# Optimization experiments

Measured on AMD Instinct MI355X. Metric: run time of the kernel, lower is better.

## Reference

```python
import jax, jax.numpy as jnp
import numpy as np

EPS = 1e-5
NUM_HEADS = 12

def _ln(x, g, b):
    m = jnp.mean(x, -1, keepdims=True)
    v = jnp.var(x, -1, keepdims=True)
    return (x - m) * jax.lax.rsqrt(v + EPS) * g + b

def setup_inputs():
    key = jax.random.key(0)
    ks = jax.random.split(key, 8)
    D, Dh = 768, 3072
    B, T, H, Wd = 8, 8, 14, 14
    def w(k, shape, scale=0.02):
        return jax.random.normal(k, shape, jnp.float32) * scale
    return dict(
        x=jax.random.normal(ks[0], (B, T * H * Wd + 1, D), jnp.float32),
        W_mq=w(ks[1], (D, D)), b_mq=jnp.zeros((D,), jnp.float32),
        W_mk=w(ks[2], (D, D)), b_mk=jnp.zeros((D,), jnp.float32),
        g1=jnp.ones((D,), jnp.float32), be1=jnp.zeros((D,), jnp.float32),
        W_qkv=w(ks[3], (3 * D, D)),
        W_proj=w(ks[4], (D, D)), b_proj=jnp.zeros((D,), jnp.float32),
        g2=jnp.ones((D,), jnp.float32), be2=jnp.zeros((D,), jnp.float32),
        W_fc1=w(ks[5], (Dh, D)), b_fc1=jnp.zeros((Dh,), jnp.float32),
        W_fc2=w(ks[6], (D, Dh)), b_fc2=jnp.zeros((D,), jnp.float32),
        B=B, T=T, H=H, Wd=Wd,
    )

def reference(x, W_mq, b_mq, W_mk, b_mk, g1, be1, W_qkv, W_proj, b_proj,
              g2, be2, W_fc1, b_fc1, W_fc2, b_fc2, B, T, H, Wd):
    D = x.shape[-1]
    nh = NUM_HEADS
    hd = D // nh
    res = x
    # cls token: (B,1,D) -> repeated per frame -> (B*T,1,D)
    cls = jnp.repeat(x[:, :1, :], T, axis=1).reshape(B * T, 1, D)
    # spatial tokens: 'b (h w t) m -> (b t) (h w) m'  (t is fastest-varying)
    xs = x[:, 1:, :].reshape(B, H * Wd, T, D).transpose(0, 2, 1, 3).reshape(B * T, H * Wd, D)
    xt = jnp.concatenate([cls, xs], axis=1)  # (BT, N=197, D)
    # learned QK-gated mask
    qm = xt @ W_mq.T + b_mq
    km = xt @ W_mk.T + b_mk
    lm = jnp.einsum('bnd,bmd->bnm', qm, km)
    lm = lm.at[:, 0, 0].set(100.0)  # force cls->cls gate open
    lm = jax.nn.sigmoid(lm)
    # attention (drop rates are 0; drop_path is identity at inference)
    xn = _ln(xt, g1, be1)
    BT, N = xt.shape[0], xt.shape[1]
    qkv = (xn @ W_qkv.T).reshape(BT, N, 3, nh, hd).transpose(2, 0, 3, 1, 4)
    q, k, v = qkv[0], qkv[1], qkv[2]  # (BT, nh, N, hd)
    attn = jax.nn.softmax(jnp.einsum('bhnd,bhmd->bhnm', q, k) * (hd ** -0.5), axis=-1)
    attn = attn * lm[:, None, :, :]  # gate attention probs with learned mask
    o = jnp.einsum('bhnm,bhmd->bhnd', attn, v).transpose(0, 2, 1, 3).reshape(BT, N, D)
    o = o @ W_proj.T + b_proj
    # gather cls back (mean over frames) and scatter tokens back
    cls_o = jnp.mean(o[:, 0, :].reshape(B, T, D), axis=1, keepdims=True)  # (B,1,D)
    xs_o = o[:, 1:, :].reshape(B, T, H * Wd, D).transpose(0, 2, 1, 3).reshape(B, H * Wd * T, D)
    y = res + jnp.concatenate([cls_o, xs_o], axis=1)
    # MLP
    h = _ln(y, g2, be2)
    h = jax.nn.gelu(h @ W_fc1.T + b_fc1, approximate=False)
    y = y + (h @ W_fc2.T + b_fc2)
    return (y, lm)
```

## Files before the change

### kernel.cpp

```cpp
#include <hip/hip_runtime.h>
#include <cstdint>

typedef _Float16 f16;
typedef f16 f16x2 __attribute__((ext_vector_type(2)));
typedef f16 f16x4 __attribute__((ext_vector_type(4)));
typedef f16 f16x8 __attribute__((ext_vector_type(8)));
typedef float f32x4 __attribute__((ext_vector_type(4)));

constexpr int D = 768;
constexpr int NTOK = 197;
constexpr int BT = 64;
constexpr int ROWS_A = BT * NTOK;
constexpr int SEQ = 1569;
constexpr int ROWS_Y = 8 * SEQ;
constexpr int DH = 3072;
constexpr int CW = 2304;
constexpr long Y_ELEMS = (long)ROWS_Y * D;

__device__ __forceinline__ void gload_lds16(const f16* g, f16* l) {
  __builtin_amdgcn_global_load_lds(
      (const __attribute__((address_space(1))) void*)g,
      (__attribute__((address_space(3))) void*)l, 16, 0, 0);
}

constexpr int DD4 = D * D / 4;
constexpr int QKV4 = CW * D / 4;
constexpr int FC4 = DH * D / 4;
constexpr int W2_TOT = QKV4 + DD4 + 2 * FC4;

__global__ __launch_bounds__(256) void cvt_weights(
    const float* __restrict__ wqkv_f, const float* __restrict__ wproj_f,
    const float* __restrict__ wfc1_f, const float* __restrict__ wfc2_f,
    f16* __restrict__ wqkv, f16* __restrict__ wproj,
    f16* __restrict__ wfc1, f16* __restrict__ wfc2) {
  const int i = blockIdx.x * 256 + threadIdx.x;
  const float* src;
  f16* dst;
  int j;
  if (i < QKV4) { src = wqkv_f; dst = wqkv; j = i; }
  else if (i < QKV4 + DD4) { src = wproj_f; dst = wproj; j = i - QKV4; }
  else if (i < QKV4 + DD4 + FC4) { src = wfc1_f; dst = wfc1; j = i - QKV4 - DD4; }
  else if (i < W2_TOT) { src = wfc2_f; dst = wfc2; j = i - QKV4 - DD4 - FC4; }
  else return;
  const float4 v = *(const float4*)(src + (size_t)j * 4);
  f16x4 o = {(f16)v.x, (f16)v.y, (f16)v.z, (f16)v.w};
  *(f16x4*)(dst + (size_t)j * 4) = o;
}

__global__ __launch_bounds__(256) void transpose2_f16(
    const float* __restrict__ wq, const float* __restrict__ wk,
    f16* __restrict__ wqT, f16* __restrict__ wkT) {
  __shared__ float tile[32][33];
  const int bid = blockIdx.x;
  const int bx = bid % 24, by = (bid / 24) % 24, z = bid / 576;
  const float* src = z ? wk : wq;
  f16* dst = z ? wkT : wqT;
  const int tx = threadIdx.x & 31, ty4 = (threadIdx.x >> 5) * 4;
#pragma unroll
  for (int r = 0; r < 4; r++)
    tile[ty4 + r][tx] = src[(size_t)(by * 32 + ty4 + r) * D + bx * 32 + tx];
  __syncthreads();
#pragma unroll
  for (int r = 0; r < 4; r++)
    dst[(size_t)(bx * 32 + ty4 + r) * D + by * 32 + tx] = (f16)tile[tx][ty4 + r];
}

__global__ __launch_bounds__(256) void weight_prep(
    const float* __restrict__ wq, const float* __restrict__ wk,
    const float* __restrict__ bq, const float* __restrict__ bk,
    float* __restrict__ rq, float* __restrict__ rk, float* __restrict__ beta) {
  const int tid = blockIdx.x * 256 + threadIdx.x;
  if (tid < D) {
    float s = 0.f;
    for (int k = 0; k < D; k++) s += wq[(size_t)k * D + tid] * bk[k];
    rq[tid] = s;
  } else if (tid < 2 * D) {
    const int i = tid - D;
    float s = 0.f;
    for (int k = 0; k < D; k++) s += wk[(size_t)k * D + i] * bq[k];
    rk[i] = s;
  }
  if (blockIdx.x == 0 && threadIdx.x < 64) {
    float c = 0.f;
    for (int k = threadIdx.x; k < D; k += 64) c += bq[k] * bk[k];
    for (int off = 32; off; off >>= 1) c += __shfl_xor(c, off);
    if (threadIdx.x == 0) beta[ROWS_A] = c;
  }
}

__global__ __launch_bounds__(192) void build_xt_xn(
    const float* __restrict__ x, const float* __restrict__ g1,
    const float* __restrict__ be1, const float* __restrict__ rq,
    const float* __restrict__ rk, f16* __restrict__ xt, f16* __restrict__ xn,
    float* __restrict__ alpha, float* __restrict__ beta) {
  const int rid = blockIdx.x;
  const int bt = rid / NTOK, n = rid % NTOK;
  const int b = bt >> 3, t = bt & 7;
  const int src = (n == 0) ? b * SEQ : b * SEQ + 1 + (n - 1) * 8 + t;
  const int tid = threadIdx.x, d0 = tid * 4;
  const float4 v = *(const float4*)(x + (size_t)src * D + d0);
  const float4 rqv = *(const float4*)(rq + d0);
  const float4 rkv = *(const float4*)(rk + d0);
  float s = v.x + v.y + v.z + v.w;
  float q = v.x * v.x + v.y * v.y + v.z * v.z + v.w * v.w;
  float a = v.x * rqv.x + v.y * rqv.y + v.z * rqv.z + v.w * rqv.w;
  float bb = v.x * rkv.x + v.y * rkv.y + v.z * rkv.z + v.w * rkv.w;
  const int lane = tid & 63, wv = tid >> 6;
  for (int off = 32; off; off >>= 1) {
    s += __shfl_xor(s, off);
    q += __shfl_xor(q, off);
    a += __shfl_xor(a, off);
    bb += __shfl_xor(bb, off);
  }
  __shared__ float red[4][3];
  if (lane == 0) { red[0][wv] = s; red[1][wv] = q; red[2][wv] = a; red[3][wv] = bb; }
  __syncthreads();
  s = red[0][0] + red[0][1] + red[0][2];
  q = red[1][0] + red[1][1] + red[1][2];
  if (tid == 0) {
    alpha[rid] = red[2][0] + red[2][1] + red[2][2];
    beta[rid] = red[3][0] + red[3][1] + red[3][2];
  }
  const float mean = s * (1.f / 768.f);
  const float var = q * (1.f / 768.f) - mean * mean;
  const float rs = rsqrtf(var + 1e-5f);
  const size_t ob = (size_t)rid * D + d0;
  f16x4 xo = {(f16)v.x, (f16)v.y, (f16)v.z, (f16)v.w};
  *(f16x4*)(xt + ob) = xo;
  const float4 gv = *(const float4*)(g1 + d0);
  const float4 bv = *(const float4*)(be1 + d0);
  f16x4 no = {(f16)((v.x - mean) * rs * gv.x + bv.x),
              (f16)((v.y - mean) * rs * gv.y + bv.y),
              (f16)((v.z - mean) * rs * gv.z + bv.z),
              (f16)((v.w - mean) * rs * gv.w + bv.w)};
  *(f16x4*)(xn + ob) = no;
}

constexpr int EPI_F16 = 0;
constexpr int EPI_F16_BIAS = 1;
constexpr int EPI_SIG = 2;
constexpr int EPI_F16_BIAS_GELU = 3;
constexpr int EPI_F32_BIAS_RES = 4;

template <int EPI, int BMT = 128, int MINW = 4>
__global__ __launch_bounds__(256, MINW) void gemm_f16(
    const f16* __restrict__ A, const f16* __restrict__ B,
    const float* __restrict__ bias, float* __restrict__ Cf,
    f16* __restrict__ Ch, const float* __restrict__ Res, int M, int N, int K,
    int lda, int ldb, int ldc, long sA, long sB, long sC) {
  constexpr int BN = 128, BK = 32;
  constexpr int MI = (BMT / 2) / 16;
  __shared__ f16 As[2][BMT][BK];
  __shared__ f16 Bs[2][BN][BK];
  const int tid = threadIdx.x;
  const int bm = blockIdx.y * BMT, bn = blockIdx.x * BN;
  const int z = blockIdx.z;
  A += (size_t)z * sA;
  B += (size_t)z * sB;
  const int lane = tid & 63, wave = tid >> 6;
  const int wm = (wave >> 1) * (BMT / 2), wn = (wave & 1) * 64;
  const int l15 = lane & 15, quad = lane >> 4;

  const int gr = lane >> 2;
  const int gc = (lane & 3) * 8;
  int a_row0 = bm + wave * 16 + gr;       if (a_row0 >= M) a_row0 = M - 1;
  int a_row1 = bm + (wave + 4) * 16 + gr; if (a_row1 >= M) a_row1 = M - 1;
  int b_row0 = bn + wave * 16 + gr;       if (b_row0 >= N) b_row0 = N - 1;
  int b_row1 = bn + (wave + 4) * 16 + gr; if (b_row1 >= N) b_row1 = N - 1;
  const f16* ap0 = A + (size_t)a_row0 * lda + gc;
  const f16* ap1 = A + (size_t)a_row1 * lda + gc;
  const f16* bp0 = B + (size_t)b_row0 * ldb + gc;
  const f16* bp1 = B + (size_t)b_row1 * ldb + gc;

  f32x4 acc[MI][4] = {};

  auto stage = [&](int buf, int k) {
    gload_lds16(ap0 + k, &As[buf][wave * 16][0]);
    if constexpr (BMT == 128)
      gload_lds16(ap1 + k, &As[buf][(wave + 4) * 16][0]);
    gload_lds16(bp0 + k, &Bs[buf][wave * 16][0]);
    gload_lds16(bp1 + k, &Bs[buf][(wave + 4) * 16][0]);
  };
  auto compute = [&](int buf) {
    f16x8 af[MI], bf[4];
#pragma unroll
    for (int i = 0; i < MI; i++)
      af[i] = *(const f16x8*)&As[buf][wm + i * 16 + l15][quad * 8];
#pragma unroll
    for (int j = 0; j < 4; j++)
      bf[j] = *(const f16x8*)&Bs[buf][wn + j * 16 + l15][quad * 8];
#pragma unroll
    for (int i = 0; i < MI; i++)
#pragma unroll
      for (int j = 0; j < 4; j++)
        acc[i][j] =
            __builtin_amdgcn_mfma_f32_16x16x32_f16(af[i], bf[j], acc[i][j], 0, 0, 0);
  };

  stage(0, 0);
  __syncthreads();
  for (int kt = 0; kt < K; kt += 2 * BK) {
    stage(1, kt + BK);
    compute(0);
    __syncthreads();
    if (kt + 2 * BK < K) stage(0, kt + 2 * BK);
    compute(1);
    __syncthreads();
  }

#pragma unroll
  for (int i = 0; i < MI; i++) {
#pragma unroll
    for (int j = 0; j < 4; j++) {
      const int col = bn + wn + j * 16 + l15;
      if (col >= N) continue;
#pragma unroll
      for (int r = 0; r < 4; r++) {
        const int row = bm + wm + i * 16 + quad * 4 + r;
        if (row >= M) continue;
        float v = acc[i][j][r];
        const size_t ci = (size_t)z * sC + (size_t)row * ldc + col;
        if constexpr (EPI == EPI_F16) {
          Ch[ci] = (f16)v;
        } else if constexpr (EPI == EPI_F16_BIAS) {
          Ch[ci] = (f16)(v + bias[col]);
        } else if constexpr (EPI == EPI_SIG) {
          v += bias[(size_t)z * NTOK + row] + Res[(size_t)z * NTOK + col] +
               Res[ROWS_A];
          if (row == 0 && col == 0) v = 100.f;
          Cf[ci] = 1.f / (1.f + __expf(-v));
        } else if constexpr (EPI == EPI_F16_BIAS_GELU) {
          const float u = v + bias[col];
          const float t = u * (0.79788456f + 0.0356774081f * u * u);
          const float e = __expf(2.f * t);
          Ch[ci] = (f16)(u * (e / (e + 1.f)));
        } else if constexpr (EPI == EPI_F32_BIAS_RES) {
          Cf[ci] = v + bias[col] + Res[ci];
        }
      }
    }
  }
}

__global__ __launch_bounds__(256, 2) void attn_kernel(
    const f16* __restrict__ qkv, const float* __restrict__ lm,
    f16* __restrict__ o) {
  __shared__ f16 Ks[208][72];
  __shared__ f16 Vt[64][232];
  __shared__ f16 Ps[4][16][40];
  const int bh = blockIdx.x;
  const int bt = bh / 12, h = bh % 12;
  const int tid = threadIdx.x, lane = tid & 63, w = tid >> 6;
  const int l15 = lane & 15, quad = lane >> 4;
  const size_t base = (size_t)bt * NTOK * CW + (size_t)h * 64;

  for (int idx = tid; idx < 208 * 8; idx += 256) {
    const int r = idx >> 3, c = (idx & 7) * 8;
    f16x8 kv = {};
    if (r < NTOK) kv = *(const f16x8*)(qkv + base + (size_t)r * CW + 768 + c);
    *(f16x8*)&Ks[r][c] = kv;
  }
  for (int cb = 0; cb < 8; cb++) {
    const int r = tid;
    if (r < NTOK) {
      const f16x8 vv = *(const f16x8*)(qkv + base + (size_t)r * CW + 1536 + cb * 8);
#pragma unroll
      for (int j = 0; j < 8; j++) Vt[cb * 8 + j][r] = vv[j];
    }
  }
  for (int idx = tid; idx < 64 * 35; idx += 256) {
    const int d = idx / 35, m = NTOK + idx % 35;
    Vt[d][m] = (f16)0.f;
  }
  __syncthreads();

  for (int nt = w; nt < 13; nt += 4) {
    const int nq = nt * 16 + l15;
    const f16* qrow = qkv + base + (size_t)nq * CW;
    const f16x8 aq0 = *(const f16x8*)(qrow + quad * 8);
    const f16x8 aq1 = *(const f16x8*)(qrow + 32 + quad * 8);
    f32x4 S[13];
#pragma unroll
    for (int t = 0; t < 13; t++) {
      const f16x8 bk0 = *(const f16x8*)&Ks[t * 16 + l15][quad * 8];
      const f16x8 bk1 = *(const f16x8*)&Ks[t * 16 + l15][32 + quad * 8];
      f32x4 s = {};
      s = __builtin_amdgcn_mfma_f32_16x16x32_f16(aq0, bk0, s, 0, 0, 0);
      s = __builtin_amdgcn_mfma_f32_16x16x32_f16(aq1, bk1, s, 0, 0, 0);
      S[t] = s;
    }
    float mx[4] = {-3e38f, -3e38f, -3e38f, -3e38f};
#pragma unroll
    for (int t = 0; t < 13; t++) {
      const int m = t * 16 + l15;
#pragma unroll
      for (int r = 0; r < 4; r++) {
        float v = (m < NTOK) ? S[t][r] * 0.125f : -1e30f;
        S[t][r] = v;
        mx[r] = fmaxf(mx[r], v);
      }
    }
#pragma unroll
    for (int off = 1; off < 16; off <<= 1)
#pragma unroll
      for (int r = 0; r < 4; r++) mx[r] = fmaxf(mx[r], __shfl_xor(mx[r], off));
    float den[4] = {0.f, 0.f, 0.f, 0.f};
#pragma unroll
    for (int t = 0; t < 13; t++)
#pragma unroll
      for (int r = 0; r < 4; r++) {
        const float e = __expf(S[t][r] - mx[r]);
        S[t][r] = e;
        den[r] += e;
      }
#pragma unroll
    for (int off = 1; off < 16; off <<= 1)
#pragma unroll
      for (int r = 0; r < 4; r++) den[r] += __shfl_xor(den[r], off);
    float inv[4];
#pragma unroll
    for (int r = 0; r < 4; r++) inv[r] = 1.f / den[r];
#pragma unroll
    for (int t = 0; t < 13; t++) {
      const int m = t * 16 + l15;
#pragma unroll
      for (int r = 0; r < 4; r++) {
        const int nrow = nt * 16 + quad * 4 + r;
        float g = 0.f;
        if (m < NTOK && nrow < NTOK)
          g = lm[((size_t)bt * NTOK + nrow) * NTOK + m];
        S[t][r] *= inv[r] * g;
      }
    }
    f32x4 O[4] = {};
    for (int c = 0; c < 7; c++) {
      __builtin_amdgcn_wave_barrier();
#pragma unroll
      for (int tt = 0; tt < 2; tt++) {
        const int t = 2 * c + tt;
#pragma unroll
        for (int r = 0; r < 4; r++) {
          const f16 pv = (t < 13) ? (f16)S[t][r] : (f16)0.f;
          Ps[w][quad * 4 + r][tt * 16 + l15] = pv;
        }
      }
      __builtin_amdgcn_wave_barrier();
      const f16x8 ap = *(const f16x8*)&Ps[w][l15][quad * 8];
#pragma unroll
      for (int dt = 0; dt < 4; dt++) {
        const f16x8 bv = *(const f16x8*)&Vt[dt * 16 + l15][c * 32 + quad * 8];
        O[dt] = __builtin_amdgcn_mfma_f32_16x16x32_f16(ap, bv, O[dt], 0, 0, 0);
      }
    }
#pragma unroll
    for (int dt = 0; dt < 4; dt++)
#pragma unroll
      for (int r = 0; r < 4; r++) {
        const int nrow = nt * 16 + quad * 4 + r;
        if (nrow < NTOK)
          o[((size_t)bt * NTOK + nrow) * D + h * 64 + dt * 16 + l15] =
              (f16)O[dt][r];
      }
  }
}

__global__ __launch_bounds__(192) void scatter_y_ln(
    const float* __restrict__ x, const f16* __restrict__ po,
    const float* __restrict__ g2, const float* __restrict__ be2,
    float* __restrict__ y, f16* __restrict__ yn) {
  const int rid = blockIdx.x;
  const int b = rid / SEQ, pos = rid % SEQ;
  const int tid = threadIdx.x, d0 = tid * 4;
  float4 v = *(const float4*)(x + (size_t)rid * D + d0);
  if (pos == 0) {
    float ax = 0, ay = 0, az = 0, aw = 0;
    for (int t = 0; t < 8; t++) {
      const f16x4 p = *(const f16x4*)(po + ((size_t)(b * 8 + t) * NTOK) * D + d0);
      ax += (float)p[0]; ay += (float)p[1]; az += (float)p[2]; aw += (float)p[3];
    }
    v.x += ax * 0.125f; v.y += ay * 0.125f; v.z += az * 0.125f; v.w += aw * 0.125f;
  } else {
    const int hw = (pos - 1) >> 3, t = (pos - 1) & 7;
    const f16x4 p =
        *(const f16x4*)(po + ((size_t)((b * 8 + t) * NTOK + 1 + hw)) * D + d0);
    v.x += (float)p[0]; v.y += (float)p[1]; v.z += (float)p[2]; v.w += (float)p[3];
  }
  *(float4*)(y + (size_t)rid * D + d0) = v;
  float s = v.x + v.y + v.z + v.w;
  float q = v.x * v.x + v.y * v.y + v.z * v.z + v.w * v.w;
  const int lane = tid & 63, wv = tid >> 6;
  for (int off = 32; off; off >>= 1) {
    s += __shfl_xor(s, off);
    q += __shfl_xor(q, off);
  }
  __shared__ float red[2][3];
  if (lane == 0) { red[0][wv] = s; red[1][wv] = q; }
  __syncthreads();
  s = red[0][0] + red[0][1] + red[0][2];
  q = red[1][0] + red[1][1] + red[1][2];
  const float mean = s * (1.f / 768.f);
  const float var = q * (1.f / 768.f) - mean * mean;
  const float rs = rsqrtf(var + 1e-5f);
  const float4 gv = *(const float4*)(g2 + d0);
  const float4 bv = *(const float4*)(be2 + d0);
  f16x4 no = {(f16)((v.x - mean) * rs * gv.x + bv.x),
              (f16)((v.y - mean) * rs * gv.y + bv.y),
              (f16)((v.z - mean) * rs * gv.z + bv.z),
              (f16)((v.w - mean) * rs * gv.w + bv.w)};
  *(f16x4*)(yn + (size_t)rid * D + d0) = no;
}

extern "C" void kernel_launch(void* const* d_in, const int* in_sizes, int n_in,
                              void* d_out, int out_size, void* d_ws,
                              size_t ws_size, hipStream_t stream) {
  const float* x = (const float*)d_in[0];
  const float* W_mq = (const float*)d_in[1];
  const float* b_mq = (const float*)d_in[2];
  const float* W_mk = (const float*)d_in[3];
  const float* b_mk = (const float*)d_in[4];
  const float* g1 = (const float*)d_in[5];
  const float* be1 = (const float*)d_in[6];
  const float* W_qkv = (const float*)d_in[7];
  const float* W_proj = (const float*)d_in[8];
  const float* b_proj = (const float*)d_in[9];
  const float* g2 = (const float*)d_in[10];
  const float* be2 = (const float*)d_in[11];
  const float* W_fc1 = (const float*)d_in[12];
  const float* b_fc1 = (const float*)d_in[13];
  const float* W_fc2 = (const float*)d_in[14];
  const float* b_fc2 = (const float*)d_in[15];

  char* ws = (char*)d_ws;
  size_t off = 0;
  auto alloc = [&](size_t bytes) {
    size_t o = off;
    off = (off + bytes + 255) & ~(size_t)255;
    return o;
  };
  const size_t o_wqT = alloc((size_t)D * D * 2);
  const size_t o_wkT = alloc((size_t)D * D * 2);
  const size_t o_wct = alloc((size_t)D * D * 2);
  const size_t o_rq = alloc((size_t)D * 4);
  const size_t o_rk = alloc((size_t)D * 4);
  const size_t o_alpha = alloc((size_t)(ROWS_A + 1) * 4);
  const size_t o_beta = alloc((size_t)(ROWS_A + 1) * 4);
  const size_t o_wqkv = alloc((size_t)CW * D * 2);
  const size_t o_wproj = alloc((size_t)D * D * 2);
  const size_t o_wfc1 = alloc((size_t)DH * D * 2);
  const size_t o_wfc2 = alloc((size_t)D * DH * 2);
  const size_t o_xt = alloc((size_t)ROWS_A * D * 2);
  const size_t o_xn = alloc((size_t)ROWS_A * D * 2);
  const size_t o_big = alloc((size_t)ROWS_A * CW * 2);
  const size_t o_po = alloc((size_t)ROWS_A * D * 2);
  const size_t o_t = o_po;
  const size_t o_qkv = o_big;
  const size_t o_o = o_xn;
  const size_t o_yn = o_xt;
  const size_t o_h = o_big;

  f16* wqT = (f16*)(ws + o_wqT);
  f16* wkT = (f16*)(ws + o_wkT);
  f16* wct = (f16*)(ws + o_wct);
  float* rq = (float*)(ws + o_rq);
  float* rk = (float*)(ws + o_rk);
  float* alpha = (float*)(ws + o_alpha);
  float* beta = (float*)(ws + o_beta);
  f16* wqkv = (f16*)(ws + o_wqkv);
  f16* wproj = (f16*)(ws + o_wproj);
  f16* wfc1 = (f16*)(ws + o_wfc1);
  f16* wfc2 = (f16*)(ws + o_wfc2);
  f16* xt = (f16*)(ws + o_xt);
  f16* xn = (f16*)(ws + o_xn);
  f16* tmat = (f16*)(ws + o_t);
  f16* qkv = (f16*)(ws + o_qkv);
  f16* oatt = (f16*)(ws + o_o);
  f16* po = (f16*)(ws + o_po);
  f16* yn = (f16*)(ws + o_yn);
  f16* h = (f16*)(ws + o_h);

  float* y_out = (float*)d_out;
  float* lm_out = (float*)d_out + Y_ELEMS;

  const dim3 blk(256);
  cvt_weights<<<dim3((W2_TOT + 255) / 256), blk, 0, stream>>>(
      W_qkv, W_proj, W_fc1, W_fc2, wqkv, wproj, wfc1, wfc2);
  transpose2_f16<<<dim3(24 * 24 * 2), blk, 0, stream>>>(W_mq, W_mk, wqT, wkT);
  weight_prep<<<dim3(6), blk, 0, stream>>>(W_mq, W_mk, b_mq, b_mk, rq, rk, beta);

  build_xt_xn<<<dim3(ROWS_A), dim3(192), 0, stream>>>(x, g1, be1, rq, rk, xt,
                                                      xn, alpha, beta);

  auto grd = [](int N_, int M_, int Z_) {
    return dim3((N_ + 127) / 128, (M_ + 127) / 128, Z_);
  };
  auto grd64 = [](int N_, int M_, int Z_) {
    return dim3((N_ + 127) / 128, (M_ + 63) / 64, Z_);
  };
  gemm_f16<EPI_F16><<<grd(D, D, 1), blk, 0, stream>>>(
      wkT, wqT, nullptr, nullptr, wct, nullptr, D, D, D, D, D, D, 0, 0, 0);
  gemm_f16<EPI_F16, 64, 5><<<grd64(D, ROWS_A, 1), blk, 0, stream>>>(
      xt, wct, nullptr, nullptr, tmat, nullptr, ROWS_A, D, D, D, D, D,
      0, 0, 0);
  gemm_f16<EPI_SIG, 64, 5><<<grd64(NTOK, NTOK, BT), blk, 0, stream>>>(
      tmat, xt, alpha, lm_out, nullptr, beta, NTOK, NTOK, D, D, D, NTOK,
      (long)NTOK * D, (long)NTOK * D, (long)NTOK * NTOK);
  gemm_f16<EPI_F16><<<grd(CW, ROWS_A, 1), blk, 0, stream>>>(
      xn, wqkv, nullptr, nullptr, qkv, nullptr, ROWS_A, CW, D, D, D, CW,
      0, 0, 0);
  attn_kernel<<<dim3(BT * 12), blk, 0, stream>>>(qkv, lm_out, oatt);
  gemm_f16<EPI_F16_BIAS, 64, 5><<<grd64(D, ROWS_A, 1), blk, 0, stream>>>(
      oatt, wproj, b_proj, nullptr, po, nullptr, ROWS_A, D, D, D, D, D,
      0, 0, 0);
  scatter_y_ln<<<dim3(ROWS_Y), dim3(192), 0, stream>>>(x, po, g2, be2, y_out, yn);
  gemm_f16<EPI_F16_BIAS_GELU><<<grd(DH, ROWS_Y, 1), blk, 0, stream>>>(
      yn, wfc1, b_fc1, nullptr, h, nullptr, ROWS_Y, DH, D, D, D, DH, 0, 0, 0);
  gemm_f16<EPI_F32_BIAS_RES, 64, 5><<<grd64(D, ROWS_Y, 1), blk, 0, stream>>>(
      h, wfc2, b_fc2, y_out, nullptr, y_out, ROWS_Y, D, DH, DH, DH, D,
      0, 0, 0);
  (void)in_sizes; (void)n_in; (void)out_size; (void)ws_size;
}
```

Before: 698.3 us.

## Unify GEMM tiles to 128x128 and add XCD-aware workgroup swizzle

Drops the 64-row tile variant so every GEMM uses 128x128 tiles with launch bounds of 3 waves. Adds an optional remap of the flat workgroup id so consecutive tiles land on the same XCD, improving L2 reuse of shared A/B panels. Larger tiles cut redundant operand loads but mean fewer workgroups for the N=768 GEMMs, which can leave CUs idle. The batched mask GEMM keeps the unswizzled mapping.

```diff
diff --git a/kernel.cpp b/kernel.cpp
--- a/kernel.cpp
+++ b/kernel.cpp
@@ -142,23 +142,29 @@
 constexpr int EPI_F16_BIAS_GELU = 3;
 constexpr int EPI_F32_BIAS_RES = 4;
 
-template <int EPI, int BMT = 128, int MINW = 4>
-__global__ __launch_bounds__(256, MINW) void gemm_f16(
+template <int EPI, bool SWZ = false>
+__global__ __launch_bounds__(256, 3) void gemm_f16(
     const f16* __restrict__ A, const f16* __restrict__ B,
     const float* __restrict__ bias, float* __restrict__ Cf,
     f16* __restrict__ Ch, const float* __restrict__ Res, int M, int N, int K,
     int lda, int ldb, int ldc, long sA, long sB, long sC) {
-  constexpr int BN = 128, BK = 32;
-  constexpr int MI = (BMT / 2) / 16;
-  __shared__ f16 As[2][BMT][BK];
+  constexpr int BM = 128, BN = 128, BK = 32;
+  __shared__ f16 As[2][BM][BK];
   __shared__ f16 Bs[2][BN][BK];
   const int tid = threadIdx.x;
-  const int bm = blockIdx.y * BMT, bn = blockIdx.x * BN;
+  int fid = blockIdx.y * gridDim.x + blockIdx.x;
+  if constexpr (SWZ) {
+    const int nwg = gridDim.x * gridDim.y;
+    const int q = nwg >> 3, r = nwg & 7;
+    const int xcd = fid & 7, p = fid >> 3;
+    fid = (xcd < r ? xcd * (q + 1) : r * (q + 1) + (xcd - r) * q) + p;
+  }
+  const int bm = (fid / gridDim.x) * BM, bn = (fid % gridDim.x) * BN;
   const int z = blockIdx.z;
   A += (size_t)z * sA;
   B += (size_t)z * sB;
   const int lane = tid & 63, wave = tid >> 6;
-  const int wm = (wave >> 1) * (BMT / 2), wn = (wave & 1) * 64;
+  const int wm = (wave >> 1) * 64, wn = (wave & 1) * 64;
   const int l15 = lane & 15, quad = lane >> 4;
 
   const int gr = lane >> 2;
@@ -172,25 +178,23 @@
   const f16* bp0 = B + (size_t)b_row0 * ldb + gc;
   const f16* bp1 = B + (size_t)b_row1 * ldb + gc;
 
-  f32x4 acc[MI][4] = {};
+  f32x4 acc[4][4] = {};
 
   auto stage = [&](int buf, int k) {
     gload_lds16(ap0 + k, &As[buf][wave * 16][0]);
-    if constexpr (BMT == 128)
-      gload_lds16(ap1 + k, &As[buf][(wave + 4) * 16][0]);
+    gload_lds16(ap1 + k, &As[buf][(wave + 4) * 16][0]);
     gload_lds16(bp0 + k, &Bs[buf][wave * 16][0]);
     gload_lds16(bp1 + k, &Bs[buf][(wave + 4) * 16][0]);
   };
   auto compute = [&](int buf) {
-    f16x8 af[MI], bf[4];
-#pragma unroll
-    for (int i = 0; i < MI; i++)
+    f16x8 af[4], bf[4];
+#pragma unroll
+    for (int i = 0; i < 4; i++) {
       af[i] = *(const f16x8*)&As[buf][wm + i * 16 + l15][quad * 8];
-#pragma unroll
-    for (int j = 0; j < 4; j++)
-      bf[j] = *(const f16x8*)&Bs[buf][wn + j * 16 + l15][quad * 8];
-#pragma unroll
-    for (int i = 0; i < MI; i++)
+      bf[i] = *(const f16x8*)&Bs[buf][wn + i * 16 + l15][quad * 8];
+    }
+#pragma unroll
+    for (int i = 0; i < 4; i++)
 #pragma unroll
       for (int j = 0; j < 4; j++)
         acc[i][j] =
@@ -209,7 +213,7 @@
   }
 
 #pragma unroll
-  for (int i = 0; i < MI; i++) {
+  for (int i = 0; i < 4; i++) {
 #pragma unroll
     for (int j = 0; j < 4; j++) {
       const int col = bn + wn + j * 16 + l15;
@@ -493,28 +497,25 @@
   auto grd = [](int N_, int M_, int Z_) {
     return dim3((N_ + 127) / 128, (M_ + 127) / 128, Z_);
   };
-  auto grd64 = [](int N_, int M_, int Z_) {
-    return dim3((N_ + 127) / 128, (M_ + 63) / 64, Z_);
-  };
-  gemm_f16<EPI_F16><<<grd(D, D, 1), blk, 0, stream>>>(
+  gemm_f16<EPI_F16, true><<<grd(D, D, 1), blk, 0, stream>>>(
       wkT, wqT, nullptr, nullptr, wct, nullptr, D, D, D, D, D, D, 0, 0, 0);
-  gemm_f16<EPI_F16, 64, 5><<<grd64(D, ROWS_A, 1), blk, 0, stream>>>(
+  gemm_f16<EPI_F16, true><<<grd(D, ROWS_A, 1), blk, 0, stream>>>(
       xt, wct, nullptr, nullptr, tmat, nullptr, ROWS_A, D, D, D, D, D,
       0, 0, 0);
-  gemm_f16<EPI_SIG, 64, 5><<<grd64(NTOK, NTOK, BT), blk, 0, stream>>>(
+  gemm_f16<EPI_SIG><<<grd(NTOK, NTOK, BT), blk, 0, stream>>>(
       tmat, xt, alpha, lm_out, nullptr, beta, NTOK, NTOK, D, D, D, NTOK,
       (long)NTOK * D, (long)NTOK * D, (long)NTOK * NTOK);
-  gemm_f16<EPI_F16><<<grd(CW, ROWS_A, 1), blk, 0, stream>>>(
+  gemm_f16<EPI_F16, true><<<grd(CW, ROWS_A, 1), blk, 0, stream>>>(
       xn, wqkv, nullptr, nullptr, qkv, nullptr, ROWS_A, CW, D, D, D, CW,
       0, 0, 0);
   attn_kernel<<<dim3(BT * 12), blk, 0, stream>>>(qkv, lm_out, oatt);
-  gemm_f16<EPI_F16_BIAS, 64, 5><<<grd64(D, ROWS_A, 1), blk, 0, stream>>>(
+  gemm_f16<EPI_F16_BIAS, true><<<grd(D, ROWS_A, 1), blk, 0, stream>>>(
       oatt, wproj, b_proj, nullptr, po, nullptr, ROWS_A, D, D, D, D, D,
       0, 0, 0);
   scatter_y_ln<<<dim3(ROWS_Y), dim3(192), 0, stream>>>(x, po, g2, be2, y_out, yn);
-  gemm_f16<EPI_F16_BIAS_GELU><<<grd(DH, ROWS_Y, 1), blk, 0, stream>>>(
+  gemm_f16<EPI_F16_BIAS_GELU, true><<<grd(DH, ROWS_Y, 1), blk, 0, stream>>>(
       yn, wfc1, b_fc1, nullptr, h, nullptr, ROWS_Y, DH, D, D, D, DH, 0, 0, 0);
-  gemm_f16<EPI_F32_BIAS_RES, 64, 5><<<grd64(D, ROWS_Y, 1), blk, 0, stream>>>(
+  gemm_f16<EPI_F32_BIAS_RES, true><<<grd(D, ROWS_Y, 1), blk, 0, stream>>>(
       h, wfc2, b_fc2, y_out, nullptr, y_out, ROWS_Y, D, DH, DH, DH, D,
       0, 0, 0);
   (void)in_sizes; (void)n_in; (void)out_size; (void)ws_size;
```

Measured after the change: 680.9 us. -2.5%, faster.
